# Optimization experiments

Measured on AMD Instinct MI355X. Metric: run time of the kernel, lower is better.

The kernel has to match this reference:

```python
import jax, jax.numpy as jnp
import numpy as np

D_MODEL = 128
EXPAND = 8
D_INNER = EXPAND * D_MODEL            # 1024
HEADDIM = D_MODEL                     # headdim = int(in_channels*8/8)
NHEADS = D_INNER // HEADDIM           # 8
D_STATE = 128
D_CONV = 4
CONV_DIM = D_INNER + 2 * D_STATE      # 1280
D_IN_PROJ = 2 * D_INNER + 2 * D_STATE + NHEADS  # 2312
EPS = 1e-5
B_SZ, SEQ = 2, 2048


def setup_inputs() -> dict:
    key = jax.random.key(0)
    ks = jax.random.split(key, 16)
    n = jax.random.normal
    dt_init = jax.random.uniform(ks[4], (NHEADS,), minval=0.001, maxval=0.1)
    return dict(
        hidden_states=n(ks[0], (B_SZ, SEQ, D_MODEL), jnp.float32),
        w_in=n(ks[1], (D_IN_PROJ, D_MODEL), jnp.float32) / np.float32(np.sqrt(D_MODEL)),
        conv_w=n(ks[2], (CONV_DIM, D_CONV), jnp.float32) / np.float32(np.sqrt(D_CONV)),
        conv_b=n(ks[3], (CONV_DIM,), jnp.float32) * 0.01,
        dt_bias=jnp.log(jnp.expm1(dt_init)),  # inverse-softplus init (official)
        A_log=jnp.log(jax.random.uniform(ks[5], (NHEADS,), minval=1.0, maxval=16.0)),
        D_skip=jnp.ones((NHEADS,), jnp.float32),
        gnorm_w=jnp.ones((D_INNER,), jnp.float32),
        w_out=n(ks[6], (D_MODEL, D_INNER), jnp.float32) / np.float32(np.sqrt(D_INNER)),
        ln1_w=jnp.ones((D_MODEL,), jnp.float32),
        ln1_b=jnp.zeros((D_MODEL,), jnp.float32),
        ln2_w=jnp.ones((D_MODEL,), jnp.float32),
        ln2_b=jnp.zeros((D_MODEL,), jnp.float32),
        mlp_w=n(ks[7], (D_MODEL, D_MODEL), jnp.float32) / np.float32(np.sqrt(D_MODEL)),
        mlp_b=jnp.zeros((D_MODEL,), jnp.float32),
    )


def _layer_norm(x, w, b):
    m = x.mean(-1, keepdims=True)
    xc = x - m
    v = (xc * xc).mean(-1, keepdims=True)
    return xc * jax.lax.rsqrt(v + EPS) * w + b


def _mixer(u, w_in, conv_w, conv_b, dt_bias, A_log, D_skip, gnorm_w, w_out):
    b, l, _ = u.shape
    zxbcdt = u @ w_in.T                                    # (b,l,2312)
    z = zxbcdt[..., :D_INNER]                              # gate
    xBC = zxbcdt[..., D_INNER:D_INNER + CONV_DIM]
    dt = jax.nn.softplus(zxbcdt[..., -NHEADS:] + dt_bias)  # (b,l,h)
    # depthwise causal conv1d + SiLU
    xc = jnp.pad(xBC.swapaxes(1, 2), ((0, 0), (0, 0), (D_CONV - 1, 0)))
    xc = jax.lax.conv_general_dilated(xc, conv_w[:, None, :], (1,), 'VALID',
                                      feature_group_count=CONV_DIM)
    xBC = jax.nn.silu((xc + conv_b[None, :, None]).swapaxes(1, 2))
    x = xBC[..., :D_INNER].reshape(b, l, NHEADS, HEADDIM)  # (b,l,h,p)
    Bm = xBC[..., D_INNER:D_INNER + D_STATE]               # (b,l,n), ngroups=1
    Cm = xBC[..., D_INNER + D_STATE:]                      # (b,l,n)
    A = -jnp.exp(A_log)                                    # (h,)
    dA = jnp.exp(dt * A)                                   # (b,l,h)

    def step(S, inp):
        dA_t, dt_t, B_t, C_t, x_t = inp
        S = S * dA_t[:, :, None, None] + jnp.einsum('bh,bhp,bn->bhpn', dt_t, x_t, B_t)
        return S, jnp.einsum('bhpn,bn->bhp', S, C_t)

    S0 = jnp.zeros((b, NHEADS, HEADDIM, D_STATE), u.dtype)
    _, ys = jax.lax.scan(step, S0, (dA.swapaxes(0, 1), dt.swapaxes(0, 1),
                                    Bm.swapaxes(0, 1), Cm.swapaxes(0, 1),
                                    x.swapaxes(0, 1)))
    y = ys.swapaxes(0, 1) + D_skip[None, None, :, None] * x  # skip connection
    y = y.reshape(b, l, D_INNER) * jax.nn.silu(z)            # gated RMSNorm
    y = y * jax.lax.rsqrt((y * y).mean(-1, keepdims=True) + EPS) * gnorm_w
    return y @ w_out.T


def reference(hidden_states, w_in, conv_w, conv_b, dt_bias, A_log, D_skip,
              gnorm_w, w_out, ln1_w, ln1_b, ln2_w, ln2_b, mlp_w, mlp_b):
    residual = hidden_states
    h = _layer_norm(residual, ln1_w, ln1_b)
    h = _mixer(h, w_in, conv_w, conv_b, dt_bias, A_log, D_skip, gnorm_w, w_out)
    residual = h + residual
    h = _layer_norm(residual, ln2_w, ln2_b)
    return h @ mlp_w.T + mlp_b
```

## Files before the change

kernel.cpp:

```cpp
#include <hip/hip_runtime.h>
#include <hip/hip_bf16.h>

#define B_SZ 2
#define SEQ 2048
#define DMODEL 128
#define DINNER 1024
#define NHEADS 8
#define HEADDIM 128
#define DSTATE 128
#define CONVDIM 1280
#define NPROJ 2304
#define NTOK (B_SZ*SEQ)
#define CHUNK 64
#define NCHUNK (SEQ/CHUNK)
#define LDT 72
#define LDU 76

using bf16_t = __hip_bfloat16;
using short8 = __attribute__((ext_vector_type(8))) short;
using short4v= __attribute__((ext_vector_type(4))) short;
using f32x4  = __attribute__((ext_vector_type(4))) float;

__device__ __forceinline__ float silu_f(float x) { return x / (1.f + expf(-x)); }
__device__ __forceinline__ float bf2f(short s) {
    unsigned u = ((unsigned)(unsigned short)s) << 16;
    return __uint_as_float(u);
}
__device__ __forceinline__ short f2bf_s(float f) {
    bf16_t h = __float2bfloat16(f);
    return *(short*)&h;
}

__global__ __launch_bounds__(128) void head_fused(
        const float* __restrict__ hidden,
        const float* __restrict__ ln1_w, const float* __restrict__ ln1_b,
        const float* __restrict__ w_in,
        const float* __restrict__ dt_bias, const float* __restrict__ A_log,
        bf16_t* __restrict__ h_bf, float* __restrict__ dtb, float* __restrict__ ldAb,
        const float* __restrict__ wa, int na, const float* __restrict__ wb, int nb,
        const float* __restrict__ wc, int nc,
        bf16_t* __restrict__ oa, bf16_t* __restrict__ ob, bf16_t* __restrict__ oc) {
    int blk = blockIdx.x;
    if (blk >= NTOK) {
        int i = ((blk - NTOK) * 128 + threadIdx.x) * 4;
        const float* src; bf16_t* dst; int base;
        if (i < na)            { src = wa; dst = oa; base = 0; }
        else if (i < na + nb)  { src = wb; dst = ob; base = na; }
        else if (i < na+nb+nc) { src = wc; dst = oc; base = na + nb; }
        else return;
        int k = i - base;
        f32x4 v = *(const f32x4*)(src + k);
        short4v o;
#pragma unroll
        for (int r = 0; r < 4; r++) o[r] = f2bf_s(v[r]);
        *(short4v*)(dst + k) = o;
        return;
    }
    int m = blk, t = threadIdx.x;
    int wave = t >> 6, lane = t & 63;
    __shared__ float sA[2], sB[2];
    __shared__ float sred[2][8];
    float v = hidden[(size_t)m*DMODEL + t];
    float s = v;
#pragma unroll
    for (int d = 1; d < 64; d <<= 1) s += __shfl_xor(s, d, 64);
    if (lane == 0) sA[wave] = s;
    __syncthreads();
    float mean = (sA[0] + sA[1]) * (1.f/128.f);
    float xc = v - mean;
    float q = xc * xc;
#pragma unroll
    for (int d = 1; d < 64; d <<= 1) q += __shfl_xor(q, d, 64);
    if (lane == 0) sB[wave] = q;
    __syncthreads();
    float var = (sB[0] + sB[1]) * (1.f/128.f);
    float o = xc * rsqrtf(var + 1e-5f) * ln1_w[t] + ln1_b[t];
    h_bf[(size_t)m*DMODEL + t] = __float2bfloat16(o);
#pragma unroll
    for (int hd = 0; hd < NHEADS; hd++) {
        float p = o * w_in[(size_t)(NPROJ + hd)*DMODEL + t];
#pragma unroll
        for (int d = 1; d < 64; d <<= 1) p += __shfl_xor(p, d, 64);
        if (lane == 0) sred[wave][hd] = p;
    }
    __syncthreads();
    if (t < NHEADS) {
        float ssum = sred[0][t] + sred[1][t] + dt_bias[t];
        float dtv = (ssum > 20.f) ? ssum : log1pf(expf(ssum));
        float Av = -expf(A_log[t]);
        dtb[m*NHEADS + t] = dtv;
        ldAb[m*NHEADS + t] = dtv * Av;
    }
}

__global__ __launch_bounds__(256) void gemm_conv(const bf16_t* __restrict__ A,
                                                 const bf16_t* __restrict__ W,
                                                 const float* __restrict__ conv_w,
                                                 const float* __restrict__ conv_b,
                                                 bf16_t* __restrict__ zbuf,
                                                 bf16_t* __restrict__ xBCb) {
    int bx = blockIdx.x, by = blockIdx.y;
    int t = threadIdx.x, wave = t >> 6, lane = t & 63;
    int lr = lane & 15, quad = lane >> 4;
    int m0 = bx * 64;
    if (by < 16) {
        int n0 = by * 64;
        int mw = m0 + wave * 16;
        f32x4 acc[4];
#pragma unroll
        for (int j = 0; j < 4; j++) acc[j] = (f32x4){0.f,0.f,0.f,0.f};
#pragma unroll
        for (int k0 = 0; k0 < 128; k0 += 32) {
            short8 a = *(const short8*)(A + (size_t)(mw + lr)*DMODEL + k0 + quad*8);
#pragma unroll
            for (int j = 0; j < 4; j++) {
                short8 b = *(const short8*)(W + (size_t)(n0 + j*16 + lr)*DMODEL + k0 + quad*8);
                acc[j] = __builtin_amdgcn_mfma_f32_16x16x32_bf16(a, b, acc[j], 0, 0, 0);
            }
        }
#pragma unroll
        for (int j = 0; j < 4; j++)
#pragma unroll
            for (int r = 0; r < 4; r++)
                zbuf[(size_t)(mw + quad*4 + r)*DINNER + n0 + j*16 + lr] = __float2bfloat16(acc[j][r]);
        return;
    }
    int cb0 = (by - 16) * 64;
    __shared__ bf16_t U[80*LDU];
    bool seqstart = ((bx & 31) == 0);
#pragma unroll
    for (int mt = 0; mt < 5; mt++) {
        if (mt == 0 && seqstart) continue;
        int rb = m0 - 16 + mt*16;
        f32x4 acc = (f32x4){0.f,0.f,0.f,0.f};
#pragma unroll
        for (int k0 = 0; k0 < 128; k0 += 32) {
            short8 a = *(const short8*)(A + (size_t)(rb + lr)*DMODEL + k0 + quad*8);
            short8 b = *(const short8*)(W + (size_t)(DINNER + cb0 + wave*16 + lr)*DMODEL + k0 + quad*8);
            acc = __builtin_amdgcn_mfma_f32_16x16x32_bf16(a, b, acc, 0, 0, 0);
        }
#pragma unroll
        for (int r = 0; r < 4; r++)
            U[(mt*16 + quad*4 + r)*LDU + wave*16 + lr] = __float2bfloat16(acc[r]);
    }
    __syncthreads();
    int c4 = (t & 15) * 4;
    int tl0 = (t >> 4) * 4;
    float bias[4]; f32x4 wv[4];
#pragma unroll
    for (int j = 0; j < 4; j++) {
        bias[j] = conv_b[cb0 + c4 + j];
        wv[j] = *(const f32x4*)(conv_w + (cb0 + c4 + j)*4);
    }
    int lbase = m0 & (SEQ - 1);
#pragma unroll
    for (int it = 0; it < 4; it++) {
        int tl = tl0 + it;
        int l = lbase + tl;
        float accv[4] = {bias[0], bias[1], bias[2], bias[3]};
#pragma unroll
        for (int k = 0; k < 4; k++) {
            int ll = l - 3 + k;
            if (ll >= 0) {
                short4v u = *(const short4v*)&U[(13 + tl + k)*LDU + c4];
#pragma unroll
                for (int j = 0; j < 4; j++) accv[j] += bf2f(u[j]) * wv[j][k];
            }
        }
        short4v res;
#pragma unroll
        for (int j = 0; j < 4; j++) res[j] = f2bf_s(silu_f(accv[j]));
        *(short4v*)(xBCb + (size_t)(m0 + tl)*CONVDIM + cb0 + c4) = res;
    }
}

__global__ __launch_bounds__(256) void scanA_mfma(const bf16_t* __restrict__ xBCb,
                                                  const float* __restrict__ dt,
                                                  const float* __restrict__ ldA,
                                                  bf16_t* __restrict__ Sloc,
                                                  float* __restrict__ Pbuf) {
    int bid = blockIdx.x;
    int nh = bid & 1, c = (bid >> 1) & 31, hd = (bid >> 6) & 7, b = bid >> 9;
    int t = threadIdx.x, wave = t >> 6, lane = t & 63;
    int lr = lane & 15, quad = lane >> 4;
    __shared__ bf16_t XT[128*LDT];
    __shared__ bf16_t BT[64*LDT];
    __shared__ float ws[CHUNK];
    int m0tok = b*SEQ + c*CHUNK;
    int bhc = (b*NHEADS + hd)*NCHUNK + c;
    if (t < 64) {
        float L = ldA[(m0tok + t)*NHEADS + hd];
#pragma unroll
        for (int d = 1; d < 64; d <<= 1) {
            float u = __shfl_up(L, d, 64);
            if (lane >= d) L += u;
        }
        float Ltot = __shfl(L, 63, 64);
        ws[t] = expf(Ltot - L) * dt[(m0tok + t)*NHEADS + hd];
        if (t == 63 && nh == 0) Pbuf[bhc] = expf(Ltot);
    }
    __syncthreads();
    int tt = t & 63;
#pragma unroll
    for (int i = 0; i < 4; i++) {
        int pg = i*4 + (t >> 6);
        short8 xv = *(const short8*)(xBCb + (size_t)(m0tok + tt)*CONVDIM + hd*HEADDIM + pg*8);
        float w = ws[tt];
#pragma unroll
        for (int j = 0; j < 8; j++)
            XT[(pg*8 + j)*LDT + tt] = __float2bfloat16(bf2f(xv[j]) * w);
    }
#pragma unroll
    for (int i = 0; i < 2; i++) {
        int pg = i*4 + (t >> 6);
        short8 bv = *(const short8*)(xBCb + (size_t)(m0tok + tt)*CONVDIM + DINNER + nh*64 + pg*8);
#pragma unroll
        for (int j = 0; j < 8; j++) {
            short sv = bv[j];
            BT[(pg*8 + j)*LDT + tt] = *(bf16_t*)&sv;
        }
    }
    __syncthreads();
    int m0w = wave * 32;
    f32x4 acc[2][4];
#pragma unroll
    for (int mi = 0; mi < 2; mi++)
#pragma unroll
        for (int ni = 0; ni < 4; ni++) acc[mi][ni] = (f32x4){0.f,0.f,0.f,0.f};
#pragma unroll
    for (int k0 = 0; k0 < 64; k0 += 32) {
        short8 a[2];
#pragma unroll
        for (int mi = 0; mi < 2; mi++)
            a[mi] = *(const short8*)&XT[(m0w + mi*16 + lr)*LDT + k0 + quad*8];
#pragma unroll
        for (int ni = 0; ni < 4; ni++) {
            short8 bb = *(const short8*)&BT[(ni*16 + lr)*LDT + k0 + quad*8];
#pragma unroll
            for (int mi = 0; mi < 2; mi++)
                acc[mi][ni] = __builtin_amdgcn_mfma_f32_16x16x32_bf16(a[mi], bb, acc[mi][ni], 0, 0, 0);
        }
    }
    bf16_t* outp = Sloc + (size_t)bhc * 16384;
#pragma unroll
    for (int mi = 0; mi < 2; mi++)
#pragma unroll
        for (int ni = 0; ni < 4; ni++)
#pragma unroll
            for (int r = 0; r < 4; r++) {
                int p = m0w + mi*16 + quad*4 + r;
                int n = nh*64 + ni*16 + lr;
                outp[p*128 + n] = __float2bfloat16(acc[mi][ni][r]);
            }
}

__global__ __launch_bounds__(256) void scanB(const bf16_t* __restrict__ Sloc,
                                             bf16_t* __restrict__ Sini,
                                             const float* __restrict__ Pbuf) {
    int bid = blockIdx.x;
    int bh = bid >> 5, slice = bid & 31;
    int t = threadIdx.x;
    int off = slice*512 + t*2;
    size_t base = (size_t)bh * NCHUNK * 16384;
    float run0 = 0.f, run1 = 0.f;
    for (int cc = 0; cc < NCHUNK; cc++) {
        unsigned raw = *(const unsigned*)(Sloc + base + (size_t)cc*16384 + off);
        float P = Pbuf[bh*NCHUNK + cc];
        unsigned o0 = (unsigned)(unsigned short)f2bf_s(run0);
        unsigned o1 = (unsigned)(unsigned short)f2bf_s(run1);
        *(unsigned*)(Sini + base + (size_t)cc*16384 + off) = o0 | (o1 << 16);
        run0 = run0*P + bf2f((short)(raw & 0xffff));
        run1 = run1*P + bf2f((short)(raw >> 16));
    }
}

__global__ __launch_bounds__(256) void scanC_mfma(const bf16_t* __restrict__ xBCb,
                                                  const float* __restrict__ dt,
                                                  const float* __restrict__ ldA,
                                                  const bf16_t* __restrict__ Sini,
                                                  const float* __restrict__ Dskip,
                                                  float* __restrict__ ybuf) {
    int bid = blockIdx.x;
    int ph = bid & 1, c = (bid >> 1) & 31, hd = (bid >> 6) & 7, b = bid >> 9;
    int t = threadIdx.x, wave = t >> 6, lane = t & 63;
    int lr = lane & 15, quad = lane >> 4;
    int pb = ph * 64;
    __shared__ bf16_t XT[64*LDT];
    __shared__ bf16_t Mlds[64*LDT];
    __shared__ float Ls[CHUNK], dts[CHUNK];
    int m0tok = b*SEQ + c*CHUNK;
    int bhc = (b*NHEADS + hd)*NCHUNK + c;
    if (t < 64) {
        float L = ldA[(m0tok + t)*NHEADS + hd];
#pragma unroll
        for (int d = 1; d < 64; d <<= 1) {
            float u = __shfl_up(L, d, 64);
            if (lane >= d) L += u;
        }
        Ls[t] = L;
        dts[t] = dt[(m0tok + t)*NHEADS + hd];
    }
    int tt = t & 63;
#pragma unroll
    for (int i = 0; i < 2; i++) {
        int pg = i*4 + (t >> 6);
        short8 xv = *(const short8*)(xBCb + (size_t)(m0tok + tt)*CONVDIM + hd*HEADDIM + pb + pg*8);
#pragma unroll
        for (int j = 0; j < 8; j++) {
            short sv = xv[j];
            XT[(pg*8 + j)*LDT + tt] = *(bf16_t*)&sv;
        }
    }
    __syncthreads();
    const bf16_t* Crow = xBCb + (size_t)m0tok*CONVDIM + DINNER + DSTATE;
    const bf16_t* Brow = xBCb + (size_t)m0tok*CONVDIM + DINNER;
    f32x4 g[4];
#pragma unroll
    for (int si = 0; si < 4; si++) g[si] = (f32x4){0.f,0.f,0.f,0.f};
#pragma unroll
    for (int k0 = 0; k0 < 128; k0 += 32) {
        short8 a = *(const short8*)(Crow + (size_t)(wave*16 + lr)*CONVDIM + k0 + quad*8);
#pragma unroll
        for (int si = 0; si < 4; si++) {
            short8 bb = *(const short8*)(Brow + (size_t)(si*16 + lr)*CONVDIM + k0 + quad*8);
            g[si] = __builtin_amdgcn_mfma_f32_16x16x32_bf16(a, bb, g[si], 0, 0, 0);
        }
    }
#pragma unroll
    for (int si = 0; si < 4; si++)
#pragma unroll
        for (int r = 0; r < 4; r++) {
            int tr = wave*16 + quad*4 + r;
            int ss = si*16 + lr;
            float v = (ss <= tr) ? g[si][r] * expf(Ls[tr] - Ls[ss]) * dts[ss] : 0.f;
            Mlds[tr*LDT + ss] = __float2bfloat16(v);
        }
    __syncthreads();
    int pw = wave * 16;
    f32x4 acc[4];
#pragma unroll
    for (int mi = 0; mi < 4; mi++) acc[mi] = (f32x4){0.f,0.f,0.f,0.f};
    const bf16_t* Sb = Sini + (size_t)bhc * 16384;
#pragma unroll
    for (int k0 = 0; k0 < 128; k0 += 32) {
        short8 aC[4];
#pragma unroll
        for (int mi = 0; mi < 4; mi++)
            aC[mi] = *(const short8*)(Crow + (size_t)(mi*16 + lr)*CONVDIM + k0 + quad*8);
        short8 bb = *(const short8*)(Sb + (size_t)(pb + pw + lr)*128 + k0 + quad*8);
#pragma unroll
        for (int mi = 0; mi < 4; mi++)
            acc[mi] = __builtin_amdgcn_mfma_f32_16x16x32_bf16(aC[mi], bb, acc[mi], 0, 0, 0);
    }
#pragma unroll
    for (int mi = 0; mi < 4; mi++) {
#pragma unroll
        for (int r = 0; r < 4; r++) acc[mi][r] *= expf(Ls[mi*16 + quad*4 + r]);
    }
#pragma unroll
    for (int k0 = 0; k0 < 64; k0 += 32) {
        short8 aM[4];
#pragma unroll
        for (int mi = 0; mi < 4; mi++)
            aM[mi] = *(const short8*)&Mlds[(mi*16 + lr)*LDT + k0 + quad*8];
        short8 bb = *(const short8*)&XT[(pw + lr)*LDT + k0 + quad*8];
#pragma unroll
        for (int mi = 0; mi < 4; mi++)
            acc[mi] = __builtin_amdgcn_mfma_f32_16x16x32_bf16(aM[mi], bb, acc[mi], 0, 0, 0);
    }
    float dsk = Dskip[hd];
#pragma unroll
    for (int mi = 0; mi < 4; mi++)
#pragma unroll
        for (int r = 0; r < 4; r++) {
            int tr = mi*16 + quad*4 + r;
            int pl = pw + lr;
            float xv = bf2f(*(const short*)&XT[pl*LDT + tr]);
            int m = m0tok + tr;
            ybuf[(size_t)m*DINNER + hd*HEADDIM + pb + pl] = acc[mi][r] + dsk*xv;
        }
}

__global__ __launch_bounds__(512) void gate_out_mlp(const float* __restrict__ ybuf,
                                                    const bf16_t* __restrict__ zbuf,
                                                    const float* __restrict__ gw,
                                                    const bf16_t* __restrict__ Wb,
                                                    const float* __restrict__ resid,
                                                    const float* __restrict__ w2,
                                                    const float* __restrict__ b2,
                                                    const bf16_t* __restrict__ Wm,
                                                    const float* __restrict__ mb,
                                                    float* __restrict__ out) {
    int blk = blockIdx.x, t = threadIdx.x;
    int tok0 = blk * 16;
    int wave = t >> 6, lane = t & 63, lr = lane & 15, quad = lane >> 4;
    __shared__ bf16_t A[16*1032];
    __shared__ float mixs[16*132];
    int tt = t >> 5, cg = t & 31;
    int ch0 = cg * 32;
    float vals[32];
    const float*  yr = ybuf + (size_t)(tok0 + tt)*DINNER + ch0;
    const bf16_t* zr = zbuf + (size_t)(tok0 + tt)*DINNER + ch0;
    float ss = 0.f;
#pragma unroll
    for (int i = 0; i < 32; i += 4) {
        f32x4 y = *(const f32x4*)(yr + i);
        short4v z = *(const short4v*)(zr + i);
#pragma unroll
        for (int r = 0; r < 4; r++) {
            float v = y[r] * silu_f(bf2f(z[r]));
            vals[i + r] = v; ss += v*v;
        }
    }
#pragma unroll
    for (int d = 1; d < 32; d <<= 1) ss += __shfl_xor(ss, d, 64);
    float rstd = rsqrtf(ss*(1.f/1024.f) + 1e-5f);
#pragma unroll
    for (int i = 0; i < 32; i += 4) {
        short4v pk;
#pragma unroll
        for (int r = 0; r < 4; r++) pk[r] = f2bf_s(vals[i+r]*rstd*gw[ch0+i+r]);
        *(short4v*)&A[tt*1032 + ch0 + i] = pk;
    }
    __syncthreads();
    int col = wave*16 + lr;
    f32x4 acc = (f32x4){0.f,0.f,0.f,0.f};
    for (int k0 = 0; k0 < 1024; k0 += 32) {
        short8 a = *(const short8*)&A[lr*1032 + k0 + quad*8];
        short8 bb = *(const short8*)(Wb + (size_t)col*DINNER + k0 + quad*8);
        acc = __builtin_amdgcn_mfma_f32_16x16x32_bf16(a, bb, acc, 0, 0, 0);
    }
#pragma unroll
    for (int r = 0; r < 4; r++)
        mixs[(quad*4 + r)*132 + col] = acc[r];
    __syncthreads();
    int ch4 = (t & 31) * 4;
    const float* rr = resid + (size_t)(tok0 + tt)*DMODEL + ch4;
    f32x4 r0 = *(const f32x4*)rr;
    float v2[4];
#pragma unroll
    for (int r = 0; r < 4; r++) v2[r] = mixs[tt*132 + ch4 + r] + r0[r];
    float s2 = 0.f, sq = 0.f;
#pragma unroll
    for (int i = 0; i < 4; i++) { s2 += v2[i]; sq += v2[i]*v2[i]; }
#pragma unroll
    for (int d = 1; d < 32; d <<= 1) { s2 += __shfl_xor(s2, d, 64); sq += __shfl_xor(sq, d, 64); }
    float mean = s2 * (1.f/128.f);
    float var  = sq * (1.f/128.f) - mean*mean;
    float rstd2 = rsqrtf(var + 1e-5f);
    {
        short4v p0;
#pragma unroll
        for (int r = 0; r < 4; r++)
            p0[r] = f2bf_s((v2[r] - mean)*rstd2*w2[ch4+r] + b2[ch4+r]);
        *(short4v*)&A[tt*136 + ch4] = p0;
    }
    __syncthreads();
    f32x4 acc2 = (f32x4){0.f,0.f,0.f,0.f};
#pragma unroll
    for (int k0 = 0; k0 < 128; k0 += 32) {
        short8 a = *(const short8*)&A[lr*136 + k0 + quad*8];
        short8 bb = *(const short8*)(Wm + (size_t)col*DMODEL + k0 + quad*8);
        acc2 = __builtin_amdgcn_mfma_f32_16x16x32_bf16(a, bb, acc2, 0, 0, 0);
    }
#pragma unroll
    for (int r = 0; r < 4; r++)
        out[(size_t)(tok0 + quad*4 + r)*DMODEL + col] = acc2[r] + mb[col];
}

extern "C" void kernel_launch(void* const* d_in, const int* in_sizes, int n_in,
                              void* d_out, int out_size, void* d_ws, size_t ws_size,
                              hipStream_t stream) {
    const float* hidden  = (const float*)d_in[0];
    const float* w_in    = (const float*)d_in[1];
    const float* conv_w  = (const float*)d_in[2];
    const float* conv_b  = (const float*)d_in[3];
    const float* dt_bias = (const float*)d_in[4];
    const float* A_log   = (const float*)d_in[5];
    const float* D_skip  = (const float*)d_in[6];
    const float* gnorm_w = (const float*)d_in[7];
    const float* w_out   = (const float*)d_in[8];
    const float* ln1_w   = (const float*)d_in[9];
    const float* ln1_b   = (const float*)d_in[10];
    const float* ln2_w   = (const float*)d_in[11];
    const float* ln2_b   = (const float*)d_in[12];
    const float* mlp_w   = (const float*)d_in[13];
    const float* mlp_b   = (const float*)d_in[14];
    float* out = (float*)d_out;

    char* ws = (char*)d_ws;
    size_t off = 0;
    auto alloc = [&](size_t bytes) -> void* {
        void* p = ws + off;
        off = (off + bytes + 255) & ~(size_t)255;
        return p;
    };
    bf16_t* h_bf   = (bf16_t*)alloc((size_t)NTOK*DMODEL*2);
    bf16_t* w_in_bf= (bf16_t*)alloc((size_t)NPROJ*DMODEL*2);
    bf16_t* w_out_bf=(bf16_t*)alloc((size_t)DMODEL*DINNER*2);
    bf16_t* mlp_bf = (bf16_t*)alloc((size_t)DMODEL*DMODEL*2);
    bf16_t* zbuf   = (bf16_t*)alloc((size_t)NTOK*DINNER*2);
    bf16_t* xBCb   = (bf16_t*)alloc((size_t)NTOK*CONVDIM*2);
    float*  dtb    = (float*) alloc((size_t)NTOK*NHEADS*4);
    float*  ldAb   = (float*) alloc((size_t)NTOK*NHEADS*4);
    bf16_t* Sloc   = (bf16_t*)alloc((size_t)B_SZ*NHEADS*NCHUNK*16384*2);
    bf16_t* Sini   = (bf16_t*)alloc((size_t)B_SZ*NHEADS*NCHUNK*16384*2);
    float*  Pbuf   = (float*) alloc((size_t)B_SZ*NHEADS*NCHUNK*4);
    float*  ybuf   = (float*) alloc((size_t)NTOK*DINNER*4);
    (void)ws_size; (void)in_sizes; (void)n_in; (void)out_size;

    {
        int na = NPROJ*DMODEL, nb = DMODEL*DINNER, nc = DMODEL*DMODEL;
        int castBlocks = (na + nb + nc) / 4 / 128;
        head_fused<<<NTOK + castBlocks, 128, 0, stream>>>(
            hidden, ln1_w, ln1_b, w_in, dt_bias, A_log, h_bf, dtb, ldAb,
            w_in, na, w_out, nb, mlp_w, nc, w_in_bf, w_out_bf, mlp_bf);
    }
    gemm_conv<<<dim3(64, 36), 256, 0, stream>>>(h_bf, w_in_bf, conv_w, conv_b, zbuf, xBCb);
    scanA_mfma<<<1024, 256, 0, stream>>>(xBCb, dtb, ldAb, Sloc, Pbuf);
    scanB<<<512, 256, 0, stream>>>(Sloc, Sini, Pbuf);
    scanC_mfma<<<1024, 256, 0, stream>>>(xBCb, dtb, ldAb, Sini, D_skip, ybuf);
    gate_out_mlp<<<NTOK/16, 512, 0, stream>>>(ybuf, zbuf, gnorm_w, w_out_bf,
                                              hidden, ln2_w, ln2_b, mlp_bf, mlp_b, out);
}
```

Before: 183.4 us.

## Fuse LayerNorm, dt projection and weight casts into input-projection GEMM; store y as bf16

Removes the separate head_fused kernel. The GEMM+conv kernel now computes LayerNorm per 64-token tile (with a 16-row halo) into shared memory, converts w_in from fp32 to bf16 on the fly, and uses extra block rows to compute dt/dA and to cast w_out/mlp_w. The scan output buffer y is also stored as bf16 instead of fp32, halving that round trip. This saves one launch and the h_bf/w_in_bf traffic, at the cost of redundant LayerNorm work per column block, fp32 weight reads inside the GEMM, and lower precision for y.

```diff
diff --git a/kernel.cpp b/kernel.cpp
--- a/kernel.cpp
+++ b/kernel.cpp
@@ -15,6 +15,8 @@
 #define NCHUNK (SEQ/CHUNK)
 #define LDT 72
 #define LDU 76
+#define NB (DMODEL*DINNER)
+#define NC (DMODEL*DMODEL)
 
 using bf16_t = __hip_bfloat16;
 using short8 = __attribute__((ext_vector_type(8))) short;
@@ -30,94 +32,150 @@
     bf16_t h = __float2bfloat16(f);
     return *(short*)&h;
 }
-
-__global__ __launch_bounds__(128) void head_fused(
+__device__ __forceinline__ short8 cvt8(const float* p) {
+    f32x4 w0 = *(const f32x4*)p, w1 = *(const f32x4*)(p + 4);
+    short8 o;
+#pragma unroll
+    for (int r = 0; r < 4; r++) { o[r] = f2bf_s(w0[r]); o[4+r] = f2bf_s(w1[r]); }
+    return o;
+}
+
+__global__ __launch_bounds__(256) void gemm_conv_ln(
         const float* __restrict__ hidden,
+        const float* __restrict__ w_in,
         const float* __restrict__ ln1_w, const float* __restrict__ ln1_b,
-        const float* __restrict__ w_in,
+        const float* __restrict__ conv_w, const float* __restrict__ conv_b,
         const float* __restrict__ dt_bias, const float* __restrict__ A_log,
-        bf16_t* __restrict__ h_bf, float* __restrict__ dtb, float* __restrict__ ldAb,
-        const float* __restrict__ wa, int na, const float* __restrict__ wb, int nb,
-        const float* __restrict__ wc, int nc,
-        bf16_t* __restrict__ oa, bf16_t* __restrict__ ob, bf16_t* __restrict__ oc) {
-    int blk = blockIdx.x;
-    if (blk >= NTOK) {
-        int i = ((blk - NTOK) * 128 + threadIdx.x) * 4;
-        const float* src; bf16_t* dst; int base;
-        if (i < na)            { src = wa; dst = oa; base = 0; }
-        else if (i < na + nb)  { src = wb; dst = ob; base = na; }
-        else if (i < na+nb+nc) { src = wc; dst = oc; base = na + nb; }
-        else return;
-        int k = i - base;
-        f32x4 v = *(const f32x4*)(src + k);
-        short4v o;
-#pragma unroll
-        for (int r = 0; r < 4; r++) o[r] = f2bf_s(v[r]);
-        *(short4v*)(dst + k) = o;
-        return;
-    }
-    int m = blk, t = threadIdx.x;
-    int wave = t >> 6, lane = t & 63;
-    __shared__ float sA[2], sB[2];
-    __shared__ float sred[2][8];
-    float v = hidden[(size_t)m*DMODEL + t];
-    float s = v;
-#pragma unroll
-    for (int d = 1; d < 64; d <<= 1) s += __shfl_xor(s, d, 64);
-    if (lane == 0) sA[wave] = s;
-    __syncthreads();
-    float mean = (sA[0] + sA[1]) * (1.f/128.f);
-    float xc = v - mean;
-    float q = xc * xc;
-#pragma unroll
-    for (int d = 1; d < 64; d <<= 1) q += __shfl_xor(q, d, 64);
-    if (lane == 0) sB[wave] = q;
-    __syncthreads();
-    float var = (sB[0] + sB[1]) * (1.f/128.f);
-    float o = xc * rsqrtf(var + 1e-5f) * ln1_w[t] + ln1_b[t];
-    h_bf[(size_t)m*DMODEL + t] = __float2bfloat16(o);
-#pragma unroll
-    for (int hd = 0; hd < NHEADS; hd++) {
-        float p = o * w_in[(size_t)(NPROJ + hd)*DMODEL + t];
-#pragma unroll
-        for (int d = 1; d < 64; d <<= 1) p += __shfl_xor(p, d, 64);
-        if (lane == 0) sred[wave][hd] = p;
-    }
-    __syncthreads();
-    if (t < NHEADS) {
-        float ssum = sred[0][t] + sred[1][t] + dt_bias[t];
-        float dtv = (ssum > 20.f) ? ssum : log1pf(expf(ssum));
-        float Av = -expf(A_log[t]);
-        dtb[m*NHEADS + t] = dtv;
-        ldAb[m*NHEADS + t] = dtv * Av;
-    }
-}
-
-__global__ __launch_bounds__(256) void gemm_conv(const bf16_t* __restrict__ A,
-                                                 const bf16_t* __restrict__ W,
-                                                 const float* __restrict__ conv_w,
-                                                 const float* __restrict__ conv_b,
-                                                 bf16_t* __restrict__ zbuf,
-                                                 bf16_t* __restrict__ xBCb) {
+        const float* __restrict__ w_out, const float* __restrict__ mlp_w,
+        bf16_t* __restrict__ zbuf, bf16_t* __restrict__ xBCb,
+        float* __restrict__ dtb, float* __restrict__ ldAb,
+        bf16_t* __restrict__ w_out_bf, bf16_t* __restrict__ mlp_bf) {
     int bx = blockIdx.x, by = blockIdx.y;
     int t = threadIdx.x, wave = t >> 6, lane = t & 63;
     int lr = lane & 15, quad = lane >> 4;
+
+    if (by == 36 || by == 37) {
+        int tid = ((by - 36)*64 + bx)*256 + t;
+        for (int e4 = tid; e4 < (NB + NC)/4; e4 += 128*256) {
+            int e = e4*4;
+            const float* src; bf16_t* dst; int k;
+            if (e < NB) { src = w_out; dst = w_out_bf; k = e; }
+            else        { src = mlp_w; dst = mlp_bf;   k = e - NB; }
+            f32x4 v = *(const f32x4*)(src + k);
+            short4v o;
+#pragma unroll
+            for (int r = 0; r < 4; r++) o[r] = f2bf_s(v[r]);
+            *(short4v*)(dst + k) = o;
+        }
+        return;
+    }
+
+    __shared__ __align__(16) char smem[39680];
+    float* sLw   = (float*)(smem + 33792);
+    float* sLb   = (float*)(smem + 34304);
+    float* meanv = (float*)(smem + 34816);
+    float* rstdv = (float*)(smem + 35136);
     int m0 = bx * 64;
+    if (t < 128) { sLw[t] = ln1_w[t]; sLb[t] = ln1_b[t]; }
+
+    if (by == 38) {
+        float* hid = (float*)smem;
+        float* wdt = (float*)(smem + 35456);
+        for (int i = t; i < 8*128; i += 256) {
+            int hd = i >> 7, k = i & 127;
+            wdt[hd*132 + k] = w_in[(size_t)(NPROJ + hd)*DMODEL + k];
+        }
+        for (int i = t; i < 64*32; i += 256) {
+            int row = i >> 5, c4 = (i & 31)*4;
+            *(f32x4*)&hid[row*132 + c4] = *(const f32x4*)(hidden + (size_t)(m0 + row)*DMODEL + c4);
+        }
+        __syncthreads();
+#pragma unroll
+        for (int i = 0; i < 16; i++) {
+            int row = wave + 4*i;
+            float v0 = hid[row*132 + lane], v1 = hid[row*132 + 64 + lane];
+            float s = v0 + v1;
+#pragma unroll
+            for (int d = 1; d < 64; d <<= 1) s += __shfl_xor(s, d, 64);
+            float mean = s * (1.f/128.f);
+            float xc0 = v0 - mean, xc1 = v1 - mean;
+            float q = xc0*xc0 + xc1*xc1;
+#pragma unroll
+            for (int d = 1; d < 64; d <<= 1) q += __shfl_xor(q, d, 64);
+            if (lane == 0) { meanv[row] = mean; rstdv[row] = rsqrtf(q*(1.f/128.f) + 1e-5f); }
+        }
+        __syncthreads();
+#pragma unroll
+        for (int pi = 0; pi < 2; pi++) {
+            int pair = pi*256 + t;
+            int tok = pair >> 3, hd = pair & 7;
+            float mean = meanv[tok], rstd = rstdv[tok];
+            float acc = 0.f;
+            for (int k = 0; k < 128; k++) {
+                float o = (hid[tok*132 + k] - mean)*rstd*sLw[k] + sLb[k];
+                acc += o * wdt[hd*132 + k];
+            }
+            float ssum = acc + dt_bias[hd];
+            float dtv = (ssum > 20.f) ? ssum : log1pf(expf(ssum));
+            float Av = -expf(A_log[hd]);
+            dtb[(m0 + tok)*NHEADS + hd]  = dtv;
+            ldAb[(m0 + tok)*NHEADS + hd] = dtv * Av;
+        }
+        return;
+    }
+
+    bf16_t* A = (bf16_t*)smem;
+    int r0 = m0 - 16;
+#pragma unroll
+    for (int i = 0; i < 20; i++) {
+        int row = wave + 4*i;
+        int gr = r0 + row;
+        float v0 = 0.f, v1 = 0.f;
+        if (gr >= 0) {
+            v0 = hidden[(size_t)gr*DMODEL + lane];
+            v1 = hidden[(size_t)gr*DMODEL + 64 + lane];
+        }
+        float s = v0 + v1;
+#pragma unroll
+        for (int d = 1; d < 64; d <<= 1) s += __shfl_xor(s, d, 64);
+        float mean = s * (1.f/128.f);
+        float xc0 = v0 - mean, xc1 = v1 - mean;
+        float q = xc0*xc0 + xc1*xc1;
+#pragma unroll
+        for (int d = 1; d < 64; d <<= 1) q += __shfl_xor(q, d, 64);
+        if (lane == 0) { meanv[row] = mean; rstdv[row] = rsqrtf(q*(1.f/128.f) + 1e-5f); }
+    }
+    __syncthreads();
+    for (int i = t; i < 80*32; i += 256) {
+        int row = i >> 5, c4 = (i & 31)*4;
+        int gr = r0 + row;
+        f32x4 h = (gr >= 0) ? *(const f32x4*)(hidden + (size_t)gr*DMODEL + c4)
+                            : (f32x4){0.f,0.f,0.f,0.f};
+        float mean = meanv[row], rstd = rstdv[row];
+        short4v o;
+#pragma unroll
+        for (int r = 0; r < 4; r++)
+            o[r] = f2bf_s((h[r] - mean)*rstd*sLw[c4 + r] + sLb[c4 + r]);
+        *(short4v*)&A[row*132 + c4] = o;
+    }
+    __syncthreads();
+
     if (by < 16) {
         int n0 = by * 64;
-        int mw = m0 + wave * 16;
+        int arow = 16 + wave*16 + lr;
         f32x4 acc[4];
 #pragma unroll
         for (int j = 0; j < 4; j++) acc[j] = (f32x4){0.f,0.f,0.f,0.f};
 #pragma unroll
         for (int k0 = 0; k0 < 128; k0 += 32) {
-            short8 a = *(const short8*)(A + (size_t)(mw + lr)*DMODEL + k0 + quad*8);
+            short8 av = *(const short8*)&A[arow*132 + k0 + quad*8];
 #pragma unroll
             for (int j = 0; j < 4; j++) {
-                short8 b = *(const short8*)(W + (size_t)(n0 + j*16 + lr)*DMODEL + k0 + quad*8);
-                acc[j] = __builtin_amdgcn_mfma_f32_16x16x32_bf16(a, b, acc[j], 0, 0, 0);
+                short8 bv = cvt8(w_in + (size_t)(n0 + j*16 + lr)*DMODEL + k0 + quad*8);
+                acc[j] = __builtin_amdgcn_mfma_f32_16x16x32_bf16(av, bv, acc[j], 0, 0, 0);
             }
         }
+        int mw = m0 + wave*16;
 #pragma unroll
         for (int j = 0; j < 4; j++)
 #pragma unroll
@@ -125,19 +183,19 @@
                 zbuf[(size_t)(mw + quad*4 + r)*DINNER + n0 + j*16 + lr] = __float2bfloat16(acc[j][r]);
         return;
     }
+
     int cb0 = (by - 16) * 64;
-    __shared__ bf16_t U[80*LDU];
+    bf16_t* U = (bf16_t*)(smem + 21120);
     bool seqstart = ((bx & 31) == 0);
 #pragma unroll
     for (int mt = 0; mt < 5; mt++) {
         if (mt == 0 && seqstart) continue;
-        int rb = m0 - 16 + mt*16;
         f32x4 acc = (f32x4){0.f,0.f,0.f,0.f};
 #pragma unroll
         for (int k0 = 0; k0 < 128; k0 += 32) {
-            short8 a = *(const short8*)(A + (size_t)(rb + lr)*DMODEL + k0 + quad*8);
-            short8 b = *(const short8*)(W + (size_t)(DINNER + cb0 + wave*16 + lr)*DMODEL + k0 + quad*8);
-            acc = __builtin_amdgcn_mfma_f32_16x16x32_bf16(a, b, acc, 0, 0, 0);
+            short8 av = *(const short8*)&A[(mt*16 + lr)*132 + k0 + quad*8];
+            short8 bv = cvt8(w_in + (size_t)(DINNER + cb0 + wave*16 + lr)*DMODEL + k0 + quad*8);
+            acc = __builtin_amdgcn_mfma_f32_16x16x32_bf16(av, bv, acc, 0, 0, 0);
         }
 #pragma unroll
         for (int r = 0; r < 4; r++)
@@ -229,16 +287,16 @@
         for (int ni = 0; ni < 4; ni++) acc[mi][ni] = (f32x4){0.f,0.f,0.f,0.f};
 #pragma unroll
     for (int k0 = 0; k0 < 64; k0 += 32) {
-        short8 a[2];
+        short8 av[2];
 #pragma unroll
         for (int mi = 0; mi < 2; mi++)
-            a[mi] = *(const short8*)&XT[(m0w + mi*16 + lr)*LDT + k0 + quad*8];
+            av[mi] = *(const short8*)&XT[(m0w + mi*16 + lr)*LDT + k0 + quad*8];
 #pragma unroll
         for (int ni = 0; ni < 4; ni++) {
             short8 bb = *(const short8*)&BT[(ni*16 + lr)*LDT + k0 + quad*8];
 #pragma unroll
             for (int mi = 0; mi < 2; mi++)
-                acc[mi][ni] = __builtin_amdgcn_mfma_f32_16x16x32_bf16(a[mi], bb, acc[mi][ni], 0, 0, 0);
+                acc[mi][ni] = __builtin_amdgcn_mfma_f32_16x16x32_bf16(av[mi], bb, acc[mi][ni], 0, 0, 0);
         }
     }
     bf16_t* outp = Sloc + (size_t)bhc * 16384;
@@ -279,7 +337,7 @@
                                                   const float* __restrict__ ldA,
                                                   const bf16_t* __restrict__ Sini,
                                                   const float* __restrict__ Dskip,
-                                                  float* __restrict__ ybuf) {
+                                                  bf16_t* __restrict__ ybuf) {
     int bid = blockIdx.x;
     int ph = bid & 1, c = (bid >> 1) & 31, hd = (bid >> 6) & 7, b = bid >> 9;
     int t = threadIdx.x, wave = t >> 6, lane = t & 63;
@@ -319,11 +377,11 @@
     for (int si = 0; si < 4; si++) g[si] = (f32x4){0.f,0.f,0.f,0.f};
 #pragma unroll
     for (int k0 = 0; k0 < 128; k0 += 32) {
-        short8 a = *(const short8*)(Crow + (size_t)(wave*16 + lr)*CONVDIM + k0 + quad*8);
+        short8 av = *(const short8*)(Crow + (size_t)(wave*16 + lr)*CONVDIM + k0 + quad*8);
 #pragma unroll
         for (int si = 0; si < 4; si++) {
             short8 bb = *(const short8*)(Brow + (size_t)(si*16 + lr)*CONVDIM + k0 + quad*8);
-            g[si] = __builtin_amdgcn_mfma_f32_16x16x32_bf16(a, bb, g[si], 0, 0, 0);
+            g[si] = __builtin_amdgcn_mfma_f32_16x16x32_bf16(av, bb, g[si], 0, 0, 0);
         }
     }
 #pragma unroll
@@ -377,11 +435,11 @@
             int pl = pw + lr;
             float xv = bf2f(*(const short*)&XT[pl*LDT + tr]);
             int m = m0tok + tr;
-            ybuf[(size_t)m*DINNER + hd*HEADDIM + pb + pl] = acc[mi][r] + dsk*xv;
-        }
-}
-
-__global__ __launch_bounds__(512) void gate_out_mlp(const float* __restrict__ ybuf,
+            ybuf[(size_t)m*DINNER + hd*HEADDIM + pb + pl] = __float2bfloat16(acc[mi][r] + dsk*xv);
+        }
+}
+
+__global__ __launch_bounds__(512) void gate_out_mlp(const bf16_t* __restrict__ ybuf,
                                                     const bf16_t* __restrict__ zbuf,
                                                     const float* __restrict__ gw,
                                                     const bf16_t* __restrict__ Wb,
@@ -399,16 +457,16 @@
     int tt = t >> 5, cg = t & 31;
     int ch0 = cg * 32;
     float vals[32];
-    const float*  yr = ybuf + (size_t)(tok0 + tt)*DINNER + ch0;
+    const bf16_t* yr = ybuf + (size_t)(tok0 + tt)*DINNER + ch0;
     const bf16_t* zr = zbuf + (size_t)(tok0 + tt)*DINNER + ch0;
     float ss = 0.f;
 #pragma unroll
     for (int i = 0; i < 32; i += 4) {
-        f32x4 y = *(const f32x4*)(yr + i);
+        short4v y = *(const short4v*)(yr + i);
         short4v z = *(const short4v*)(zr + i);
 #pragma unroll
         for (int r = 0; r < 4; r++) {
-            float v = y[r] * silu_f(bf2f(z[r]));
+            float v = bf2f(y[r]) * silu_f(bf2f(z[r]));
             vals[i + r] = v; ss += v*v;
         }
     }
@@ -495,8 +553,6 @@
         off = (off + bytes + 255) & ~(size_t)255;
         return p;
     };
-    bf16_t* h_bf   = (bf16_t*)alloc((size_t)NTOK*DMODEL*2);
-    bf16_t* w_in_bf= (bf16_t*)alloc((size_t)NPROJ*DMODEL*2);
     bf16_t* w_out_bf=(bf16_t*)alloc((size_t)DMODEL*DINNER*2);
     bf16_t* mlp_bf = (bf16_t*)alloc((size_t)DMODEL*DMODEL*2);
     bf16_t* zbuf   = (bf16_t*)alloc((size_t)NTOK*DINNER*2);
@@ -506,17 +562,12 @@
     bf16_t* Sloc   = (bf16_t*)alloc((size_t)B_SZ*NHEADS*NCHUNK*16384*2);
     bf16_t* Sini   = (bf16_t*)alloc((size_t)B_SZ*NHEADS*NCHUNK*16384*2);
     float*  Pbuf   = (float*) alloc((size_t)B_SZ*NHEADS*NCHUNK*4);
-    float*  ybuf   = (float*) alloc((size_t)NTOK*DINNER*4);
+    bf16_t* ybuf   = (bf16_t*)alloc((size_t)NTOK*DINNER*2);
     (void)ws_size; (void)in_sizes; (void)n_in; (void)out_size;
 
-    {
-        int na = NPROJ*DMODEL, nb = DMODEL*DINNER, nc = DMODEL*DMODEL;
-        int castBlocks = (na + nb + nc) / 4 / 128;
-        head_fused<<<NTOK + castBlocks, 128, 0, stream>>>(
-            hidden, ln1_w, ln1_b, w_in, dt_bias, A_log, h_bf, dtb, ldAb,
-            w_in, na, w_out, nb, mlp_w, nc, w_in_bf, w_out_bf, mlp_bf);
-    }
-    gemm_conv<<<dim3(64, 36), 256, 0, stream>>>(h_bf, w_in_bf, conv_w, conv_b, zbuf, xBCb);
+    gemm_conv_ln<<<dim3(64, 39), 256, 0, stream>>>(
+        hidden, w_in, ln1_w, ln1_b, conv_w, conv_b, dt_bias, A_log,
+        w_out, mlp_w, zbuf, xBCb, dtb, ldAb, w_out_bf, mlp_bf);
     scanA_mfma<<<1024, 256, 0, stream>>>(xBCb, dtb, ldAb, Sloc, Pbuf);
     scanB<<<512, 256, 0, stream>>>(Sloc, Sini, Pbuf);
     scanC_mfma<<<1024, 256, 0, stream>>>(xBCb, dtb, ldAb, Sini, D_skip, ybuf);
```

Result: slower. 225.4 us (+22.9%).
